# Optimization experiments

Hardware: AMD Instinct MI355X
Metric: run time of the kernel (lower is better)

Reference implementation:

```python
import jax, jax.numpy as jnp
import numpy as np

NEG_INF = -1e9  # matches masked_fill value in the torch source


def setup_inputs() -> dict:
    key0 = jax.random.key(0)
    kq, kk, kv, km = jax.random.split(key0, 4)
    B, H, S, D = 2, 12, 2048, 64
    query = jax.random.normal(kq, (B, H, S, D), dtype=jnp.float32)
    key = jax.random.normal(kk, (B, H, S, D), dtype=jnp.float32)
    value = jax.random.normal(kv, (B, H, S, D), dtype=jnp.float32)
    mask = jax.random.randint(km, (B, S, S), 0, 2, dtype=jnp.int32)
    return {"query": query, "key": key, "value": value, "mask": mask}


def reference(query, key, value, mask):
    # query/key/value: [B, H, S, D]; mask: [B, S, S] (0 = masked out)
    d = key.shape[-1]
    scale = 1.0 / np.sqrt(d).astype(np.float32)
    # attn scores: [B, H, Sq, Sk]
    attn = jnp.einsum("bhqd,bhkd->bhqk", query * scale, key)
    m = mask[:, None, :, :]  # broadcast over heads, mirrors mask.unsqueeze(1)
    attn = jnp.where(m == 0, jnp.float32(NEG_INF), attn)
    attn = jax.nn.softmax(attn, axis=-1)
    # dropout_ratio = 0.0 -> identity
    out = jnp.einsum("bhqk,bhkd->bhqd", attn, value)
    return out
```

## Files before the change

### kernel.cpp

```cpp
#include <hip/hip_runtime.h>

#define SQ 2048
#define DH 64
#define NH 12
#define NBH 24

typedef __attribute__((ext_vector_type(8))) short short8;
typedef __attribute__((ext_vector_type(16))) float f32x16;

union U8 { uint4 u; short8 s; };

__device__ __forceinline__ unsigned short f2bf(float x) {
  union { float f; unsigned u; } v; v.f = x;
  return (unsigned short)((v.u + 0x7FFFu + ((v.u >> 16) & 1u)) >> 16);
}

__device__ __forceinline__ unsigned pk2(float a, float b) {
  unsigned ua = __builtin_bit_cast(unsigned, a) + 0x8000u;
  unsigned ub = __builtin_bit_cast(unsigned, b) + 0x8000u;
  return __builtin_amdgcn_perm(ub, ua, 0x07060302);
}

__device__ __forceinline__ void gload_lds16(const void* g, void* l) {
  __builtin_amdgcn_global_load_lds(
      (const __attribute__((address_space(1))) unsigned*)g,
      (__attribute__((address_space(3))) unsigned*)l, 16, 0, 0);
}

__device__ __forceinline__ int sw23(int x) {
  return (x & 19) | ((x & 4) << 1) | ((x & 8) >> 1);
}

__global__ __launch_bounds__(256) void prep_all(
    const float* __restrict__ Q, const float* __restrict__ K,
    const float* __restrict__ V, const int* __restrict__ M,
    unsigned short* __restrict__ Qb, unsigned short* __restrict__ Kb,
    unsigned short* __restrict__ Vt, unsigned* __restrict__ mbits) {
  const int bid = blockIdx.x, tid = threadIdx.x;
  if (bid < 3072) {
    int i = bid * 256 + tid;
    float4 q = ((const float4*)Q)[i];
    float4 k = ((const float4*)K)[i];
    const float sc = 0.125f * 1.44269504f;
    ushort4 qo, ko;
    qo.x = f2bf(q.x * sc); qo.y = f2bf(q.y * sc);
    qo.z = f2bf(q.z * sc); qo.w = f2bf(q.w * sc);
    ko.x = f2bf(k.x); ko.y = f2bf(k.y); ko.z = f2bf(k.z); ko.w = f2bf(k.w);
    ((ushort4*)Qb)[i] = qo;
    ((ushort4*)Kb)[i] = ko;
  } else if (bid < 3840) {
    __shared__ float T[64 * 65];
    int bx = bid - 3072;
    int bh = bx >> 5, st = bx & 31;
    int s0 = st * 64;
    int c4 = (tid & 15) * 4, r0 = tid >> 4;
#pragma unroll
    for (int it = 0; it < 4; ++it) {
      int r = r0 + 16 * it;
      float4 v = *(const float4*)(V + ((size_t)(bh * SQ + s0 + r)) * DH + c4);
      T[r * 65 + c4 + 0] = v.x; T[r * 65 + c4 + 1] = v.y;
      T[r * 65 + c4 + 2] = v.z; T[r * 65 + c4 + 3] = v.w;
    }
    __syncthreads();
#pragma unroll
    for (int it = 0; it < 2; ++it) {
      int cc = tid + 256 * it;
      int d = cc >> 3, c8 = (cc & 7) * 8;
      short8 o;
#pragma unroll
      for (int j = 0; j < 8; ++j) o[j] = (short)f2bf(T[(c8 + j) * 65 + d]);
      *(short8*)(Vt + ((size_t)(bh * 64 + d)) * SQ + s0 + c8) = o;
    }
  } else {
    int w = tid >> 6, lane = tid & 63;
    int row = (bid - 3840) * 4 + w;
    const int* mrow = M + (size_t)row * SQ;
    unsigned long long out = 0;
#pragma unroll
    for (int j = 0; j < 32; ++j) {
      int mv = mrow[j * 64 + lane];
      unsigned long long bits = __ballot(mv != 0);
      if (lane == j) out = bits;
    }
    if (lane < 32)
      ((unsigned long long*)mbits)[(size_t)row * 32 + lane] = out;
  }
}

__global__ __launch_bounds__(256, 3) void attn_kernel(
    const unsigned short* __restrict__ Qb, const unsigned short* __restrict__ Kb,
    const unsigned short* __restrict__ Vt, const unsigned* __restrict__ mbits,
    float* __restrict__ O0, float* __restrict__ O1, float* __restrict__ Lp) {
  __shared__ uint4 FIFO[2][16][64];

  const int bx = blockIdx.x;
  const int bh = bx % NBH;
  const int rest = bx / NBH;
  const int qt = rest & 15, ks = rest >> 4;
  const int b = bh / NH;
  const int tid = threadIdx.x;
  const int lane = tid & 63, w = tid >> 6;
  const int n = lane & 31, h = lane >> 5;
  const int qrow = qt * 128 + w * 32 + n;
  const int k0 = ks * (SQ / 2);

  short8 qf[4];
#pragma unroll
  for (int s = 0; s < 4; ++s)
    qf[s] = *(const short8*)(Qb + ((size_t)(bh * SQ + qrow)) * DH + 16 * s + 8 * h);

  const unsigned short* gp[4];
  if (w < 2) {
#pragma unroll
    for (int j = 0; j < 4; ++j) {
      int c = 4 * w + j;
      int row = k0 + 32 * (c >> 2) + sw23(n);
      gp[j] = Kb + ((size_t)bh * SQ + row) * DH + 16 * (c & 3) + 8 * h;
    }
  } else {
#pragma unroll
    for (int j = 0; j < 4; ++j) {
      int cc = 4 * (w - 2) + j;
      gp[j] = Vt + ((size_t)bh * DH + 32 * (cc >> 2) + n) * SQ + k0 + 16 * (cc & 3) + 8 * h;
    }
  }
  const int gstride = (w < 2) ? 64 * DH : 64;
  const int chunk0 = w * 4;

  const unsigned long long* mp =
      (const unsigned long long*)mbits + ((size_t)b * SQ + qrow) * 32 + (k0 >> 6);

  short8 ones;
#pragma unroll
  for (int j = 0; j < 8; ++j) ones[j] = (short)0x3F80;

  f32x16 acc0 = {0,0,0,0,0,0,0,0,0,0,0,0,0,0,0,0};
  f32x16 acc1 = {0,0,0,0,0,0,0,0,0,0,0,0,0,0,0,0};
  f32x16 sumac = {0,0,0,0,0,0,0,0,0,0,0,0,0,0,0,0};

#pragma unroll
  for (int j = 0; j < 4; ++j) {
    gload_lds16(gp[j], &FIFO[0][chunk0 + j][0]);
    gp[j] += gstride;
  }
  __syncthreads();

  for (int nt = 0; nt < 16; ++nt) {
    const int cur = nt & 1;
    if (nt < 15) {
#pragma unroll
      for (int j = 0; j < 4; ++j) {
        gload_lds16(gp[j], &FIFO[1 - cur][chunk0 + j][0]);
        gp[j] += gstride;
      }
    }
    unsigned long long mg = *mp; ++mp;

    short8 pb[2][2];
#pragma unroll
    for (int u = 0; u < 2; ++u) {
      f32x16 st = {0,0,0,0,0,0,0,0,0,0,0,0,0,0,0,0};
#pragma unroll
      for (int s = 0; s < 4; ++s) {
        U8 kf; kf.u = FIFO[cur][4 * u + s][lane];
        st = __builtin_amdgcn_mfma_f32_32x32x16_bf16(kf.s, qf[s], st, 0, 0, 0);
      }
      unsigned blo = (unsigned)(mg >> (8 * (4 * u + h))) & 0xFFu;
      unsigned bhi = (unsigned)(mg >> (8 * (4 * u + 2 + h))) & 0xFFu;
      float p[16];
#pragma unroll
      for (int j = 0; j < 16; ++j) {
        float e = __builtin_amdgcn_exp2f(st[j]);
        unsigned byt = (j < 8) ? blo : bhi;
        p[j] = ((byt >> (j & 7)) & 1u) ? e : 0.f;
      }
      U8 x0, x1;
      x0.u = (uint4){pk2(p[0], p[1]), pk2(p[2], p[3]), pk2(p[4], p[5]), pk2(p[6], p[7])};
      x1.u = (uint4){pk2(p[8], p[9]), pk2(p[10], p[11]), pk2(p[12], p[13]), pk2(p[14], p[15])};
      pb[u][0] = x0.s;
      pb[u][1] = x1.s;
    }

#pragma unroll
    for (int t = 0; t < 4; ++t) {
      short8 pf = pb[t >> 1][t & 1];
      sumac = __builtin_amdgcn_mfma_f32_32x32x16_bf16(ones, pf, sumac, 0, 0, 0);
      U8 v0; v0.u = FIFO[cur][8 + t][lane];
      acc0 = __builtin_amdgcn_mfma_f32_32x32x16_bf16(v0.s, pf, acc0, 0, 0, 0);
      U8 v1; v1.u = FIFO[cur][12 + t][lane];
      acc1 = __builtin_amdgcn_mfma_f32_32x32x16_bf16(v1.s, pf, acc1, 0, 0, 0);
    }

    __syncthreads();
  }

  float* op = (ks ? O1 : O0) + ((size_t)(bh * SQ + qrow)) * DH;
#pragma unroll
  for (int dt = 0; dt < 2; ++dt) {
    f32x16 A = dt ? acc1 : acc0;
#pragma unroll
    for (int a = 0; a < 4; ++a) {
      float4 o = {A[4 * a], A[4 * a + 1], A[4 * a + 2], A[4 * a + 3]};
      *(float4*)(op + 32 * dt + 8 * a + 4 * h) = o;
    }
  }
  if (lane < 32) Lp[(size_t)ks * NBH * SQ + bh * SQ + qrow] = sumac[0];
}

__global__ __launch_bounds__(256) void combine(float* __restrict__ Out,
                                               const float* __restrict__ O1,
                                               const float* __restrict__ Lp) {
  int i = blockIdx.x * 256 + threadIdx.x;
  float4 a = ((const float4*)Out)[i];
  float4 bb = ((const float4*)O1)[i];
  int q = i >> 4;
  float inv = __builtin_amdgcn_rcpf(Lp[q] + Lp[NBH * SQ + q]);
  float4 o = {(a.x + bb.x) * inv, (a.y + bb.y) * inv,
              (a.z + bb.z) * inv, (a.w + bb.w) * inv};
  ((float4*)Out)[i] = o;
}

extern "C" void kernel_launch(void* const* d_in, const int* in_sizes, int n_in,
                              void* d_out, int out_size, void* d_ws, size_t ws_size,
                              hipStream_t stream) {
  const float* Q = (const float*)d_in[0];
  const float* K = (const float*)d_in[1];
  const float* V = (const float*)d_in[2];
  const int*   M = (const int*)d_in[3];
  float* Out = (float*)d_out;

  size_t NB = (size_t)NBH * SQ * DH;
  unsigned short* Qb = (unsigned short*)d_ws;
  unsigned short* Kb = Qb + NB;
  unsigned short* Vt = Kb + NB;
  unsigned* mbits = (unsigned*)(Vt + NB);
  float* O1 = (float*)(mbits + (size_t)2 * SQ * 64);
  float* Lp = O1 + NB;

  prep_all<<<4864, 256, 0, stream>>>(Q, K, V, M, Qb, Kb, Vt, mbits);
  attn_kernel<<<NBH * 16 * 2, 256, 0, stream>>>(Qb, Kb, Vt, mbits, Out, O1, Lp);
  combine<<<(int)(NB / 4 / 256), 256, 0, stream>>>(Out, O1, Lp);
}
```

Measured before the change: 156.8 us.

## Split keys four ways with bf16 partials and MFMA priority hints

Result: slower. 164.6 us (+5.0%).

```diff
diff --git a/kernel.cpp b/kernel.cpp
--- a/kernel.cpp
+++ b/kernel.cpp
@@ -4,6 +4,10 @@
 #define DH 64
 #define NH 12
 #define NBH 24
+#define NKS 4
+#define KITERS (SQ / NKS / 64)
+
+#define NBEL ((size_t)NBH * SQ * DH)
 
 typedef __attribute__((ext_vector_type(8))) short short8;
 typedef __attribute__((ext_vector_type(16))) float f32x16;
@@ -87,10 +91,11 @@
   }
 }
 
-__global__ __launch_bounds__(256, 3) void attn_kernel(
+__global__ __launch_bounds__(256, 4) void attn_kernel(
     const unsigned short* __restrict__ Qb, const unsigned short* __restrict__ Kb,
     const unsigned short* __restrict__ Vt, const unsigned* __restrict__ mbits,
-    float* __restrict__ O0, float* __restrict__ O1, float* __restrict__ Lp) {
+    unsigned short* __restrict__ P01, unsigned short* __restrict__ P23,
+    float* __restrict__ Lp) {
   __shared__ uint4 FIFO[2][16][64];
 
   const int bx = blockIdx.x;
@@ -102,7 +107,7 @@
   const int lane = tid & 63, w = tid >> 6;
   const int n = lane & 31, h = lane >> 5;
   const int qrow = qt * 128 + w * 32 + n;
-  const int k0 = ks * (SQ / 2);
+  const int k0 = ks * (SQ / NKS);
 
   short8 qf[4];
 #pragma unroll
@@ -145,9 +150,9 @@
   }
   __syncthreads();
 
-  for (int nt = 0; nt < 16; ++nt) {
+  for (int nt = 0; nt < KITERS; ++nt) {
     const int cur = nt & 1;
-    if (nt < 15) {
+    if (nt < KITERS - 1) {
 #pragma unroll
       for (int j = 0; j < 4; ++j) {
         gload_lds16(gp[j], &FIFO[1 - cur][chunk0 + j][0]);
@@ -160,11 +165,13 @@
 #pragma unroll
     for (int u = 0; u < 2; ++u) {
       f32x16 st = {0,0,0,0,0,0,0,0,0,0,0,0,0,0,0,0};
+      __builtin_amdgcn_s_setprio(1);
 #pragma unroll
       for (int s = 0; s < 4; ++s) {
         U8 kf; kf.u = FIFO[cur][4 * u + s][lane];
         st = __builtin_amdgcn_mfma_f32_32x32x16_bf16(kf.s, qf[s], st, 0, 0, 0);
       }
+      __builtin_amdgcn_s_setprio(0);
       unsigned blo = (unsigned)(mg >> (8 * (4 * u + h))) & 0xFFu;
       unsigned bhi = (unsigned)(mg >> (8 * (4 * u + 2 + h))) & 0xFFu;
       float p[16];
@@ -181,6 +188,7 @@
       pb[u][1] = x1.s;
     }
 
+    __builtin_amdgcn_s_setprio(1);
 #pragma unroll
     for (int t = 0; t < 4; ++t) {
       short8 pf = pb[t >> 1][t & 1];
@@ -190,33 +198,47 @@
       U8 v1; v1.u = FIFO[cur][12 + t][lane];
       acc1 = __builtin_amdgcn_mfma_f32_32x32x16_bf16(v1.s, pf, acc1, 0, 0, 0);
     }
+    __builtin_amdgcn_s_setprio(0);
 
     __syncthreads();
   }
 
-  float* op = (ks ? O1 : O0) + ((size_t)(bh * SQ + qrow)) * DH;
+  unsigned short* base = (ks < 2) ? P01 : P23;
+  const int ksl = ks & 1;
 #pragma unroll
   for (int dt = 0; dt < 2; ++dt) {
     f32x16 A = dt ? acc1 : acc0;
 #pragma unroll
     for (int a = 0; a < 4; ++a) {
-      float4 o = {A[4 * a], A[4 * a + 1], A[4 * a + 2], A[4 * a + 3]};
-      *(float4*)(op + 32 * dt + 8 * a + 4 * h) = o;
+      size_t eo = ((size_t)(bh * SQ + qrow)) * DH + 32 * dt + 8 * a + 4 * h;
+      uint2 o = {pk2(A[4 * a], A[4 * a + 1]), pk2(A[4 * a + 2], A[4 * a + 3])};
+      *(uint2*)(base + 2 * eo + 4 * ksl) = o;
     }
   }
   if (lane < 32) Lp[(size_t)ks * NBH * SQ + bh * SQ + qrow] = sumac[0];
 }
 
+__device__ __forceinline__ float bflo(unsigned w) {
+  return __builtin_bit_cast(float, w << 16);
+}
+__device__ __forceinline__ float bfhi(unsigned w) {
+  return __builtin_bit_cast(float, w & 0xFFFF0000u);
+}
+
 __global__ __launch_bounds__(256) void combine(float* __restrict__ Out,
-                                               const float* __restrict__ O1,
+                                               const unsigned short* __restrict__ P23,
                                                const float* __restrict__ Lp) {
   int i = blockIdx.x * 256 + threadIdx.x;
-  float4 a = ((const float4*)Out)[i];
-  float4 bb = ((const float4*)O1)[i];
   int q = i >> 4;
-  float inv = __builtin_amdgcn_rcpf(Lp[q] + Lp[NBH * SQ + q]);
-  float4 o = {(a.x + bb.x) * inv, (a.y + bb.y) * inv,
-              (a.z + bb.z) * inv, (a.w + bb.w) * inv};
+  float l = Lp[q] + Lp[NBH * SQ + q] + Lp[2 * NBH * SQ + q] + Lp[3 * NBH * SQ + q];
+  float inv = __builtin_amdgcn_rcpf(l);
+  uint4 a01 = ((const uint4*)Out)[i];
+  uint4 a23 = ((const uint4*)P23)[i];
+  float s0 = bflo(a01.x) + bflo(a01.z) + bflo(a23.x) + bflo(a23.z);
+  float s1 = bfhi(a01.x) + bfhi(a01.z) + bfhi(a23.x) + bfhi(a23.z);
+  float s2 = bflo(a01.y) + bflo(a01.w) + bflo(a23.y) + bflo(a23.w);
+  float s3 = bfhi(a01.y) + bfhi(a01.w) + bfhi(a23.y) + bfhi(a23.w);
+  float4 o = {s0 * inv, s1 * inv, s2 * inv, s3 * inv};
   ((float4*)Out)[i] = o;
 }
 
@@ -229,15 +251,16 @@
   const int*   M = (const int*)d_in[3];
   float* Out = (float*)d_out;
 
-  size_t NB = (size_t)NBH * SQ * DH;
+  size_t NB = NBEL;
   unsigned short* Qb = (unsigned short*)d_ws;
   unsigned short* Kb = Qb + NB;
   unsigned short* Vt = Kb + NB;
   unsigned* mbits = (unsigned*)(Vt + NB);
-  float* O1 = (float*)(mbits + (size_t)2 * SQ * 64);
-  float* Lp = O1 + NB;
+  unsigned short* P23 = (unsigned short*)(mbits + (size_t)2 * SQ * 64);
+  float* Lp = (float*)(P23 + 2 * NB);
+  unsigned short* P01 = (unsigned short*)Out;
 
   prep_all<<<4864, 256, 0, stream>>>(Q, K, V, M, Qb, Kb, Vt, mbits);
-  attn_kernel<<<NBH * 16 * 2, 256, 0, stream>>>(Qb, Kb, Vt, mbits, Out, O1, Lp);
-  combine<<<(int)(NB / 4 / 256), 256, 0, stream>>>(Out, O1, Lp);
-}
+  attn_kernel<<<NBH * 16 * NKS, 256, 0, stream>>>(Qb, Kb, Vt, mbits, P01, P23, Lp);
+  combine<<<(int)(NB / 4 / 256), 256, 0, stream>>>(Out, P23, Lp);
+}
```

## Triple-buffer K/V LDS pipeline with manual vmcnt waits and MFMA priority

Applied to the files above, without the earlier changes.

Measured after the change: 158.2 us. No clear change (+0.9%).

```diff
diff --git a/kernel.cpp b/kernel.cpp
--- a/kernel.cpp
+++ b/kernel.cpp
@@ -4,6 +4,8 @@
 #define DH 64
 #define NH 12
 #define NBH 24
+#define NKS 2
+#define KITERS (SQ / NKS / 64)
 
 typedef __attribute__((ext_vector_type(8))) short short8;
 typedef __attribute__((ext_vector_type(16))) float f32x16;
@@ -91,7 +93,7 @@
     const unsigned short* __restrict__ Qb, const unsigned short* __restrict__ Kb,
     const unsigned short* __restrict__ Vt, const unsigned* __restrict__ mbits,
     float* __restrict__ O0, float* __restrict__ O1, float* __restrict__ Lp) {
-  __shared__ uint4 FIFO[2][16][64];
+  __shared__ uint4 FIFO[3][16][64];
 
   const int bx = blockIdx.x;
   const int bh = bx % NBH;
@@ -102,7 +104,7 @@
   const int lane = tid & 63, w = tid >> 6;
   const int n = lane & 31, h = lane >> 5;
   const int qrow = qt * 128 + w * 32 + n;
-  const int k0 = ks * (SQ / 2);
+  const int k0 = ks * (SQ / NKS);
 
   short8 qf[4];
 #pragma unroll
@@ -143,28 +145,43 @@
     gload_lds16(gp[j], &FIFO[0][chunk0 + j][0]);
     gp[j] += gstride;
   }
-  __syncthreads();
-
-  for (int nt = 0; nt < 16; ++nt) {
-    const int cur = nt & 1;
-    if (nt < 15) {
+#pragma unroll
+  for (int j = 0; j < 4; ++j) {
+    gload_lds16(gp[j], &FIFO[1][chunk0 + j][0]);
+    gp[j] += gstride;
+  }
+
+  for (int nt = 0; nt < KITERS; ++nt) {
+    const int cur = nt % 3;
+    if (nt < KITERS - 1) {
+      asm volatile("s_waitcnt vmcnt(4)" ::: "memory");
+    } else {
+      asm volatile("s_waitcnt vmcnt(0)" ::: "memory");
+    }
+    __builtin_amdgcn_s_barrier();
+
+    if (nt < KITERS - 2) {
+      const int nbuf = (nt + 2) % 3;
 #pragma unroll
       for (int j = 0; j < 4; ++j) {
-        gload_lds16(gp[j], &FIFO[1 - cur][chunk0 + j][0]);
+        gload_lds16(gp[j], &FIFO[nbuf][chunk0 + j][0]);
         gp[j] += gstride;
       }
     }
+
     unsigned long long mg = *mp; ++mp;
 
     short8 pb[2][2];
 #pragma unroll
     for (int u = 0; u < 2; ++u) {
       f32x16 st = {0,0,0,0,0,0,0,0,0,0,0,0,0,0,0,0};
+      __builtin_amdgcn_s_setprio(1);
 #pragma unroll
       for (int s = 0; s < 4; ++s) {
         U8 kf; kf.u = FIFO[cur][4 * u + s][lane];
         st = __builtin_amdgcn_mfma_f32_32x32x16_bf16(kf.s, qf[s], st, 0, 0, 0);
       }
+      __builtin_amdgcn_s_setprio(0);
       unsigned blo = (unsigned)(mg >> (8 * (4 * u + h))) & 0xFFu;
       unsigned bhi = (unsigned)(mg >> (8 * (4 * u + 2 + h))) & 0xFFu;
       float p[16];
@@ -181,6 +198,7 @@
       pb[u][1] = x1.s;
     }
 
+    __builtin_amdgcn_s_setprio(1);
 #pragma unroll
     for (int t = 0; t < 4; ++t) {
       short8 pf = pb[t >> 1][t & 1];
@@ -190,8 +208,7 @@
       U8 v1; v1.u = FIFO[cur][12 + t][lane];
       acc1 = __builtin_amdgcn_mfma_f32_32x32x16_bf16(v1.s, pf, acc1, 0, 0, 0);
     }
-
-    __syncthreads();
+    __builtin_amdgcn_s_setprio(0);
   }
 
   float* op = (ks ? O1 : O0) + ((size_t)(bh * SQ + qrow)) * DH;
```

## Split each block's KV tile across wave pairs with LDS reduction of partial outputs

Applied to the files above, without the earlier changes.

Measured after the change: 185.2 us. +18.1%, slower.

```diff
diff --git a/kernel.cpp b/kernel.cpp
--- a/kernel.cpp
+++ b/kernel.cpp
@@ -4,6 +4,8 @@
 #define DH 64
 #define NH 12
 #define NBH 24
+#define NKS 2
+#define KITERS (SQ / NKS / 64)
 
 typedef __attribute__((ext_vector_type(8))) short short8;
 typedef __attribute__((ext_vector_type(16))) float f32x16;
@@ -87,7 +89,7 @@
   }
 }
 
-__global__ __launch_bounds__(256, 3) void attn_kernel(
+__global__ __launch_bounds__(256, 4) void attn_kernel(
     const unsigned short* __restrict__ Qb, const unsigned short* __restrict__ Kb,
     const unsigned short* __restrict__ Vt, const unsigned* __restrict__ mbits,
     float* __restrict__ O0, float* __restrict__ O1, float* __restrict__ Lp) {
@@ -96,13 +98,14 @@
   const int bx = blockIdx.x;
   const int bh = bx % NBH;
   const int rest = bx / NBH;
-  const int qt = rest & 15, ks = rest >> 4;
+  const int qt = rest & 31, ks = rest >> 5;
   const int b = bh / NH;
   const int tid = threadIdx.x;
   const int lane = tid & 63, w = tid >> 6;
   const int n = lane & 31, h = lane >> 5;
-  const int qrow = qt * 128 + w * 32 + n;
-  const int k0 = ks * (SQ / 2);
+  const int qh = w & 1, kh = w >> 1;
+  const int qrow = qt * 64 + qh * 32 + n;
+  const int k0 = ks * (SQ / NKS);
 
   short8 qf[4];
 #pragma unroll
@@ -127,8 +130,8 @@
   const int gstride = (w < 2) ? 64 * DH : 64;
   const int chunk0 = w * 4;
 
-  const unsigned long long* mp =
-      (const unsigned long long*)mbits + ((size_t)b * SQ + qrow) * 32 + (k0 >> 6);
+  const unsigned* mp32 =
+      mbits + ((size_t)b * SQ + qrow) * 64 + (k0 >> 5) + kh;
 
   short8 ones;
 #pragma unroll
@@ -145,66 +148,79 @@
   }
   __syncthreads();
 
-  for (int nt = 0; nt < 16; ++nt) {
+  for (int nt = 0; nt < KITERS; ++nt) {
     const int cur = nt & 1;
-    if (nt < 15) {
+    if (nt < KITERS - 1) {
 #pragma unroll
       for (int j = 0; j < 4; ++j) {
         gload_lds16(gp[j], &FIFO[1 - cur][chunk0 + j][0]);
         gp[j] += gstride;
       }
     }
-    unsigned long long mg = *mp; ++mp;
-
-    short8 pb[2][2];
-#pragma unroll
-    for (int u = 0; u < 2; ++u) {
-      f32x16 st = {0,0,0,0,0,0,0,0,0,0,0,0,0,0,0,0};
-#pragma unroll
-      for (int s = 0; s < 4; ++s) {
-        U8 kf; kf.u = FIFO[cur][4 * u + s][lane];
-        st = __builtin_amdgcn_mfma_f32_32x32x16_bf16(kf.s, qf[s], st, 0, 0, 0);
+    unsigned mgw = *mp32; mp32 += 2;
+
+    f32x16 st = {0,0,0,0,0,0,0,0,0,0,0,0,0,0,0,0};
+#pragma unroll
+    for (int s = 0; s < 4; ++s) {
+      U8 kf; kf.u = FIFO[cur][4 * kh + s][lane];
+      st = __builtin_amdgcn_mfma_f32_32x32x16_bf16(kf.s, qf[s], st, 0, 0, 0);
+    }
+    unsigned blo = (mgw >> (8 * h)) & 0xFFu;
+    unsigned bhi = (mgw >> (16 + 8 * h)) & 0xFFu;
+    float p[16];
+#pragma unroll
+    for (int j = 0; j < 16; ++j) {
+      float e = __builtin_amdgcn_exp2f(st[j]);
+      unsigned byt = (j < 8) ? blo : bhi;
+      p[j] = ((byt >> (j & 7)) & 1u) ? e : 0.f;
+    }
+    U8 x0, x1;
+    x0.u = (uint4){pk2(p[0], p[1]), pk2(p[2], p[3]), pk2(p[4], p[5]), pk2(p[6], p[7])};
+    x1.u = (uint4){pk2(p[8], p[9]), pk2(p[10], p[11]), pk2(p[12], p[13]), pk2(p[14], p[15])};
+
+#pragma unroll
+    for (int t = 0; t < 2; ++t) {
+      short8 pf = t ? x1.s : x0.s;
+      sumac = __builtin_amdgcn_mfma_f32_32x32x16_bf16(ones, pf, sumac, 0, 0, 0);
+      U8 v0; v0.u = FIFO[cur][8 + 2 * kh + t][lane];
+      acc0 = __builtin_amdgcn_mfma_f32_32x32x16_bf16(v0.s, pf, acc0, 0, 0, 0);
+      U8 v1; v1.u = FIFO[cur][12 + 2 * kh + t][lane];
+      acc1 = __builtin_amdgcn_mfma_f32_32x32x16_bf16(v1.s, pf, acc1, 0, 0, 0);
+    }
+
+    __syncthreads();
+  }
+
+  float* SCR = (float*)FIFO;
+  if (kh == 1) {
+    float* sp = SCR + (size_t)(qh * 64 + lane) * 33;
+#pragma unroll
+    for (int j = 0; j < 16; ++j) sp[j] = acc0[j];
+#pragma unroll
+    for (int j = 0; j < 16; ++j) sp[16 + j] = acc1[j];
+    sp[32] = sumac[0];
+  }
+  __syncthreads();
+  if (kh == 0) {
+    const float* sp = SCR + (size_t)(qh * 64 + lane) * 33;
+#pragma unroll
+    for (int j = 0; j < 16; ++j) acc0[j] += sp[j];
+#pragma unroll
+    for (int j = 0; j < 16; ++j) acc1[j] += sp[16 + j];
+    float l = sumac[0] + sp[32];
+
+    float* op = (ks ? O1 : O0) + ((size_t)(bh * SQ + qrow)) * DH;
+#pragma unroll
+    for (int dt = 0; dt < 2; ++dt) {
+      f32x16 A = dt ? acc1 : acc0;
+#pragma unroll
+      for (int a = 0; a < 4; ++a) {
+        float4 o = {A[4 * a], A[4 * a + 1], A[4 * a + 2], A[4 * a + 3]};
+        *(float4*)(op + 32 * dt + 8 * a + 4 * h) = o;
       }
-      unsigned blo = (unsigned)(mg >> (8 * (4 * u + h))) & 0xFFu;
-      unsigned bhi = (unsigned)(mg >> (8 * (4 * u + 2 + h))) & 0xFFu;
-      float p[16];
-#pragma unroll
-      for (int j = 0; j < 16; ++j) {
-        float e = __builtin_amdgcn_exp2f(st[j]);
-        unsigned byt = (j < 8) ? blo : bhi;
-        p[j] = ((byt >> (j & 7)) & 1u) ? e : 0.f;
-      }
-      U8 x0, x1;
-      x0.u = (uint4){pk2(p[0], p[1]), pk2(p[2], p[3]), pk2(p[4], p[5]), pk2(p[6], p[7])};
-      x1.u = (uint4){pk2(p[8], p[9]), pk2(p[10], p[11]), pk2(p[12], p[13]), pk2(p[14], p[15])};
-      pb[u][0] = x0.s;
-      pb[u][1] = x1.s;
-    }
-
-#pragma unroll
-    for (int t = 0; t < 4; ++t) {
-      short8 pf = pb[t >> 1][t & 1];
-      sumac = __builtin_amdgcn_mfma_f32_32x32x16_bf16(ones, pf, sumac, 0, 0, 0);
-      U8 v0; v0.u = FIFO[cur][8 + t][lane];
-      acc0 = __builtin_amdgcn_mfma_f32_32x32x16_bf16(v0.s, pf, acc0, 0, 0, 0);
-      U8 v1; v1.u = FIFO[cur][12 + t][lane];
-      acc1 = __builtin_amdgcn_mfma_f32_32x32x16_bf16(v1.s, pf, acc1, 0, 0, 0);
-    }
-
-    __syncthreads();
-  }
-
-  float* op = (ks ? O1 : O0) + ((size_t)(bh * SQ + qrow)) * DH;
-#pragma unroll
-  for (int dt = 0; dt < 2; ++dt) {
-    f32x16 A = dt ? acc1 : acc0;
-#pragma unroll
-    for (int a = 0; a < 4; ++a) {
-      float4 o = {A[4 * a], A[4 * a + 1], A[4 * a + 2], A[4 * a + 3]};
-      *(float4*)(op + 32 * dt + 8 * a + 4 * h) = o;
-    }
-  }
-  if (lane < 32) Lp[(size_t)ks * NBH * SQ + bh * SQ + qrow] = sumac[0];
+    }
+    if (lane < 32) Lp[(size_t)ks * NBH * SQ + bh * SQ + qrow] = l;
+  }
 }
 
 __global__ __launch_bounds__(256) void combine(float* __restrict__ Out,
@@ -238,6 +254,6 @@
   float* Lp = O1 + NB;
 
   prep_all<<<4864, 256, 0, stream>>>(Q, K, V, M, Qb, Kb, Vt, mbits);
-  attn_kernel<<<NBH * 16 * 2, 256, 0, stream>>>(Qb, Kb, Vt, mbits, Out, O1, Lp);
+  attn_kernel<<<NBH * 32 * 2, 256, 0, stream>>>(Qb, Kb, Vt, mbits, Out, O1, Lp);
   combine<<<(int)(NB / 4 / 256), 256, 0, stream>>>(Out, O1, Lp);
 }
```
